# Optimization experiments

Hardware: AMD Instinct MI355X
Metric: run time of the kernel (lower is better)

The kernel has to match this reference:

```python
import jax, jax.numpy as jnp
import numpy as np

VOCAB = 100000
HID = 256
BATCH = 4096
TOTAL_TOKENS = 819200
BN_EPS = 1e-5


def setup_inputs() -> dict:
    key = jax.random.key(0)
    ks = jax.random.split(key, 8)
    token_ids = jax.random.randint(ks[0], (TOTAL_TOKENS,), 0, VOCAB, dtype=jnp.int64)
    segment_ids = jnp.sort(jax.random.randint(ks[1], (TOTAL_TOKENS,), 0, BATCH, dtype=jnp.int64))
    labels = jax.random.uniform(ks[2], (BATCH,), dtype=jnp.float32)
    emb = jax.random.normal(ks[3], (VOCAB, HID), dtype=jnp.float32)
    W1 = jax.random.normal(ks[4], (HID, HID), dtype=jnp.float32) * (1.0 / np.sqrt(HID))
    b1 = jnp.zeros((HID,), dtype=jnp.float32)
    gamma = jnp.ones((HID,), dtype=jnp.float32)
    beta = jnp.zeros((HID,), dtype=jnp.float32)
    W2 = jax.random.normal(ks[5], (1, HID), dtype=jnp.float32) * (1.0 / np.sqrt(HID))
    b2 = jnp.zeros((1,), dtype=jnp.float32)
    return {"token_ids": token_ids, "segment_ids": segment_ids, "labels": labels,
            "emb": emb, "W1": W1, "b1": b1, "gamma": gamma, "beta": beta,
            "W2": W2, "b2": b2}


def reference(token_ids, segment_ids, labels, emb, W1, b1, gamma, beta, W2, b2):
    # Ragged embedding gather + per-document mean (fused EmbeddingBag-mean).
    tok_emb = emb[token_ids]                                   # [T, H]
    seg_sum = jax.ops.segment_sum(tok_emb, segment_ids, num_segments=BATCH)  # [B, H]
    counts = jax.ops.segment_sum(jnp.ones((token_ids.shape[0],), tok_emb.dtype),
                                 segment_ids, num_segments=BATCH)            # [B]
    bow = seg_sum / jnp.maximum(counts, 1.0)[:, None]          # [B, H]
    # Linear -> BatchNorm1d (batch stats, biased var) -> ReLU
    h = bow @ W1.T + b1                                        # [B, H]
    mu = jnp.mean(h, axis=0)
    var = jnp.mean((h - mu) ** 2, axis=0)
    h = (h - mu) * jax.lax.rsqrt(var + BN_EPS) * gamma + beta
    h = jax.nn.relu(h)
    # Dropout in eval mode (identity) for deterministic reference.
    logits = (h @ W2.T + b2)[:, 0]                             # [B]
    # BCEWithLogitsLoss (mean), numerically stable form.
    loss = jnp.mean(jnp.maximum(logits, 0.0) - logits * labels
                    + jnp.log1p(jnp.exp(-jnp.abs(logits))))
    return (loss, logits)
```

## Files before the change

### kernel.cpp

```cpp
#include <hip/hip_runtime.h>
#include <math.h>

#define VOCAB 100000
#define HID 256
#define BATCH 4096
#define BN_EPS 1e-5f
#define TPB1 512
#define ROWS2 8

#define WS_SEGSUM 0
#define WS_COUNTS (BATCH * HID)
#define WS_COLSUM (WS_COUNTS + BATCH)
#define WS_COLSQ  (WS_COLSUM + HID)
#define WS_ZERO_FLOATS (WS_COLSQ + HID)

__global__ __launch_bounds__(256) void k1_gather_segsum(
    const int* __restrict__ token_ids, const int* __restrict__ segment_ids,
    const float* __restrict__ emb, float* __restrict__ seg_sum,
    float* __restrict__ counts, int T)
{
    __shared__ int s_tok[TPB1];
    __shared__ int s_seg[TPB1];
    const int tid  = threadIdx.x;
    const int t0   = blockIdx.x * TPB1;
    const int n    = min(TPB1, T - t0);
    if (n <= 0) return;
    for (int i = tid; i < n; i += 256) {
        s_tok[i] = token_ids[t0 + i];
        s_seg[i] = segment_ids[t0 + i];
    }
    __syncthreads();

    const int wave = tid >> 6;
    const int lane = tid & 63;
    const int per  = TPB1 / 4;
    const int start = wave * per;
    const int end   = min(start + per, n);
    if (start >= end) return;

    const float4* __restrict__ embv = reinterpret_cast<const float4*>(emb);
    float4 acc = make_float4(0.f, 0.f, 0.f, 0.f);
    int cur = s_seg[start];
    int runlen = 0;

#define K1_FLUSH() do {                                                        \
        float* p = &seg_sum[(size_t)cur * HID + lane * 4];                     \
        atomicAdd(p + 0, acc.x); atomicAdd(p + 1, acc.y);                      \
        atomicAdd(p + 2, acc.z); atomicAdd(p + 3, acc.w);                      \
        if (lane == 0) atomicAdd(&counts[cur], (float)runlen);                 \
        acc = make_float4(0.f, 0.f, 0.f, 0.f); runlen = 0;                     \
    } while (0)

#define K1_PROC(ii, v) do {                                                    \
        int seg = s_seg[ii];                  \
        if (seg != cur) { K1_FLUSH(); cur = seg; }                             \
        acc.x += (v).x; acc.y += (v).y; acc.z += (v).z; acc.w += (v).w;        \
        runlen++;                                                              \
    } while (0)

    const int m4 = start + ((end - start) & ~3);
    for (int i = start; i < m4; i += 4) {
        float4 a0 = embv[(size_t)s_tok[i + 0] * (HID / 4) + lane];
        float4 a1 = embv[(size_t)s_tok[i + 1] * (HID / 4) + lane];
        float4 a2 = embv[(size_t)s_tok[i + 2] * (HID / 4) + lane];
        float4 a3 = embv[(size_t)s_tok[i + 3] * (HID / 4) + lane];
        K1_PROC(i + 0, a0);
        K1_PROC(i + 1, a1);
        K1_PROC(i + 2, a2);
        K1_PROC(i + 3, a3);
    }
    for (int i = m4; i < end; ++i) {
        float4 a = embv[(size_t)s_tok[i] * (HID / 4) + lane];
        K1_PROC(i, a);
    }
    K1_FLUSH();
#undef K1_PROC
#undef K1_FLUSH
}

__global__ __launch_bounds__(256) void k2_gemm_bn_partial(
    const float* seg_sum, const float* __restrict__ counts,
    const float* __restrict__ W1, const float* __restrict__ b1,
    float* hout, float* __restrict__ colsum, float* __restrict__ colsq,
    float* __restrict__ out)
{
    __shared__ float s_bow[ROWS2][HID];
    const int tid = threadIdx.x;
    const int b0  = blockIdx.x * ROWS2;

    if (blockIdx.x == 0 && tid == 0) out[0] = 0.f;

#pragma unroll
    for (int r = 0; r < ROWS2; ++r) {
        float c   = counts[b0 + r];
        float inv = 1.f / fmaxf(c, 1.f);
        s_bow[r][tid] = seg_sum[(size_t)(b0 + r) * HID + tid] * inv;
    }
    __syncthreads();

    const int j = tid;
    float acc[ROWS2];
    const float bj = b1[j];
#pragma unroll
    for (int r = 0; r < ROWS2; ++r) acc[r] = bj;

    const float4* W1v = reinterpret_cast<const float4*>(W1 + (size_t)j * HID);
#pragma unroll 4
    for (int k4 = 0; k4 < HID / 4; ++k4) {
        float4 w = W1v[k4];
#pragma unroll
        for (int r = 0; r < ROWS2; ++r) {
            const float4* bv = reinterpret_cast<const float4*>(&s_bow[r][0]);
            float4 bb = bv[k4];
            acc[r] = fmaf(bb.x, w.x, acc[r]);
            acc[r] = fmaf(bb.y, w.y, acc[r]);
            acc[r] = fmaf(bb.z, w.z, acc[r]);
            acc[r] = fmaf(bb.w, w.w, acc[r]);
        }
    }

    float ls = 0.f, lq = 0.f;
#pragma unroll
    for (int r = 0; r < ROWS2; ++r) {
        float v = acc[r];
        hout[(size_t)(b0 + r) * HID + j] = v;
        ls += v;
        lq += v * v;
    }
    atomicAdd(&colsum[j], ls);
    atomicAdd(&colsq[j], lq);
}

__global__ __launch_bounds__(256) void k5_bn_relu_logits_loss(
    const float* __restrict__ hmat,
    const float* __restrict__ colsum, const float* __restrict__ colsq,
    const float* __restrict__ gamma, const float* __restrict__ beta,
    const float* __restrict__ W2, const float* __restrict__ b2,
    const float* __restrict__ labels, float* __restrict__ out)
{
    __shared__ float s_loss[4];
    const int tid  = threadIdx.x;
    const int w    = tid >> 6;
    const int lane = tid & 63;
    const int b0   = blockIdx.x * 16 + w * 4;

    const int j0 = lane, j1 = lane + 64, j2 = lane + 128, j3 = lane + 192;

#define BN_SS(jj, sc, sh) \
    { float mu = colsum[jj] * (1.f / BATCH); \
      float vr = colsq[jj] * (1.f / BATCH) - mu * mu; \
      sc = gamma[jj] * rsqrtf(vr + BN_EPS); \
      sh = beta[jj] - mu * sc; }
    float sc0, sh0, sc1, sh1, sc2, sh2, sc3, sh3;
    BN_SS(j0, sc0, sh0); BN_SS(j1, sc1, sh1);
    BN_SS(j2, sc2, sh2); BN_SS(j3, sc3, sh3);
#undef BN_SS

    const float w0 = W2[j0], w1 = W2[j1], w2v = W2[j2], w3 = W2[j3];
    const float bias2 = b2[0];

    float bce_acc = 0.f;
#pragma unroll
    for (int rr = 0; rr < 4; ++rr) {
        const int b = b0 + rr;
        const float* hr = hmat + (size_t)b * HID;
        float h0 = hr[j0], h1 = hr[j1], h2 = hr[j2], h3 = hr[j3];
        float s = 0.f;
        s += fmaxf(fmaf(h0, sc0, sh0), 0.f) * w0;
        s += fmaxf(fmaf(h1, sc1, sh1), 0.f) * w1;
        s += fmaxf(fmaf(h2, sc2, sh2), 0.f) * w2v;
        s += fmaxf(fmaf(h3, sc3, sh3), 0.f) * w3;
#pragma unroll
        for (int off = 32; off > 0; off >>= 1)
            s += __shfl_down(s, off, 64);
        if (lane == 0) {
            float z = s + bias2;
            out[1 + b] = z;
            float lb = labels[b];
            bce_acc += fmaxf(z, 0.f) - z * lb + log1pf(expf(-fabsf(z)));
        }
    }
    if (lane == 0) s_loss[w] = bce_acc;
    __syncthreads();
    if (tid == 0) {
        float t = (s_loss[0] + s_loss[1]) + (s_loss[2] + s_loss[3]);
        atomicAdd(&out[0], t * (1.f / BATCH));
    }
}

extern "C" void kernel_launch(void* const* d_in, const int* in_sizes, int n_in,
                              void* d_out, int out_size, void* d_ws, size_t ws_size,
                              hipStream_t stream)
{
    const int*   token_ids   = (const int*)d_in[0];
    const int*   segment_ids = (const int*)d_in[1];
    const float* labels      = (const float*)d_in[2];
    const float* emb         = (const float*)d_in[3];
    const float* W1          = (const float*)d_in[4];
    const float* b1          = (const float*)d_in[5];
    const float* gamma       = (const float*)d_in[6];
    const float* beta        = (const float*)d_in[7];
    const float* W2          = (const float*)d_in[8];
    const float* b2          = (const float*)d_in[9];
    float* out = (float*)d_out;
    float* ws  = (float*)d_ws;

    float* seg_sum = ws + WS_SEGSUM;
    float* counts  = ws + WS_COUNTS;
    float* colsum  = ws + WS_COLSUM;
    float* colsq   = ws + WS_COLSQ;

    const int T = in_sizes[0];

    hipMemsetAsync(d_ws, 0, (size_t)WS_ZERO_FLOATS * sizeof(float), stream);

    const int g1 = (T + TPB1 - 1) / TPB1;
    k1_gather_segsum<<<g1, 256, 0, stream>>>(token_ids, segment_ids, emb,
                                             seg_sum, counts, T);
    k2_gemm_bn_partial<<<BATCH / ROWS2, 256, 0, stream>>>(
        seg_sum, counts, W1, b1, seg_sum, colsum, colsq, out);
    k5_bn_relu_logits_loss<<<BATCH / 16, 256, 0, stream>>>(
        seg_sum, colsum, colsq, gamma, beta, W2, b2, labels, out);
}
```

Baseline: 312.6 us.

## Convert embedding table to fp16 per call and gather halves; tile W1 via shared memory

Each call now runs a kernel that converts the fp32 embedding table to fp16 in workspace, and the gather reads 8-byte half rows with 8-way unrolled loads, accumulating in fp32. This halves the gather bytes per token but adds a full read of the table and a half-size write on every call. The GEMM kernel also stages W1 in transposed K-tiles in shared memory with register prefetch, replacing per-thread strided row reads. A fallback keeps the fp32 gather when the workspace is too small.

```diff
diff --git a/kernel.cpp b/kernel.cpp
--- a/kernel.cpp
+++ b/kernel.cpp
@@ -1,4 +1,5 @@
 #include <hip/hip_runtime.h>
+#include <hip/hip_fp16.h>
 #include <math.h>
 
 #define VOCAB 100000
@@ -7,23 +8,40 @@
 #define BN_EPS 1e-5f
 #define TPB1 512
 #define ROWS2 8
+#define KT 16
 
 #define WS_SEGSUM 0
 #define WS_COUNTS (BATCH * HID)
 #define WS_COLSUM (WS_COUNTS + BATCH)
 #define WS_COLSQ  (WS_COLSUM + HID)
 #define WS_ZERO_FLOATS (WS_COLSQ + HID)
-
-__global__ __launch_bounds__(256) void k1_gather_segsum(
+#define WS_EMB16_OFF_BYTES ((size_t)WS_ZERO_FLOATS * 4)
+#define WS_FP16_BYTES_NEEDED (WS_EMB16_OFF_BYTES + (size_t)VOCAB * HID * 2)
+
+__global__ __launch_bounds__(256) void k0_convert(
+    const float* __restrict__ emb, __half* __restrict__ emb16, int n4)
+{
+    int i = blockIdx.x * 256 + threadIdx.x;
+    if (i >= n4) return;
+    float4 v = reinterpret_cast<const float4*>(emb)[i];
+    __half2 a = __halves2half2(__float2half_rn(v.x), __float2half_rn(v.y));
+    __half2 b = __halves2half2(__float2half_rn(v.z), __float2half_rn(v.w));
+    uint2 o;
+    o.x = __builtin_bit_cast(unsigned int, a);
+    o.y = __builtin_bit_cast(unsigned int, b);
+    reinterpret_cast<uint2*>(emb16)[i] = o;
+}
+
+__global__ __launch_bounds__(256) void k1_gather_fp16(
     const int* __restrict__ token_ids, const int* __restrict__ segment_ids,
-    const float* __restrict__ emb, float* __restrict__ seg_sum,
+    const __half* __restrict__ emb16, float* __restrict__ seg_sum,
     float* __restrict__ counts, int T)
 {
     __shared__ int s_tok[TPB1];
     __shared__ int s_seg[TPB1];
-    const int tid  = threadIdx.x;
-    const int t0   = blockIdx.x * TPB1;
-    const int n    = min(TPB1, T - t0);
+    const int tid = threadIdx.x;
+    const int t0  = blockIdx.x * TPB1;
+    const int n   = min(TPB1, T - t0);
     if (n <= 0) return;
     for (int i = tid; i < n; i += 256) {
         s_tok[i] = token_ids[t0 + i];
@@ -38,7 +56,7 @@
     const int end   = min(start + per, n);
     if (start >= end) return;
 
-    const float4* __restrict__ embv = reinterpret_cast<const float4*>(emb);
+    const uint2* __restrict__ embv = reinterpret_cast<const uint2*>(emb16);
     float4 acc = make_float4(0.f, 0.f, 0.f, 0.f);
     int cur = s_seg[start];
     int runlen = 0;
@@ -51,8 +69,80 @@
         acc = make_float4(0.f, 0.f, 0.f, 0.f); runlen = 0;                     \
     } while (0)
 
+#define K1_PROC16(ii, u) do {                                                  \
+        int seg = s_seg[ii];                  \
+        if (seg != cur) { K1_FLUSH(); cur = seg; }                             \
+        __half2 h01 = __builtin_bit_cast(__half2, (u).x);                      \
+        __half2 h23 = __builtin_bit_cast(__half2, (u).y);                      \
+        float2 f01 = __half22float2(h01);                                      \
+        float2 f23 = __half22float2(h23);                                      \
+        acc.x += f01.x; acc.y += f01.y; acc.z += f23.x; acc.w += f23.y;        \
+        runlen++;                                                              \
+    } while (0)
+
+    const int m8 = start + ((end - start) & ~7);
+    for (int i = start; i < m8; i += 8) {
+        uint2 u0 = embv[(size_t)s_tok[i + 0] * 64 + lane];
+        uint2 u1 = embv[(size_t)s_tok[i + 1] * 64 + lane];
+        uint2 u2 = embv[(size_t)s_tok[i + 2] * 64 + lane];
+        uint2 u3 = embv[(size_t)s_tok[i + 3] * 64 + lane];
+        uint2 u4 = embv[(size_t)s_tok[i + 4] * 64 + lane];
+        uint2 u5 = embv[(size_t)s_tok[i + 5] * 64 + lane];
+        uint2 u6 = embv[(size_t)s_tok[i + 6] * 64 + lane];
+        uint2 u7 = embv[(size_t)s_tok[i + 7] * 64 + lane];
+        K1_PROC16(i + 0, u0); K1_PROC16(i + 1, u1);
+        K1_PROC16(i + 2, u2); K1_PROC16(i + 3, u3);
+        K1_PROC16(i + 4, u4); K1_PROC16(i + 5, u5);
+        K1_PROC16(i + 6, u6); K1_PROC16(i + 7, u7);
+    }
+    for (int i = m8; i < end; ++i) {
+        uint2 u = embv[(size_t)s_tok[i] * 64 + lane];
+        K1_PROC16(i, u);
+    }
+    K1_FLUSH();
+#undef K1_PROC16
+#undef K1_FLUSH
+}
+
+__global__ __launch_bounds__(256) void k1_gather_fp32(
+    const int* __restrict__ token_ids, const int* __restrict__ segment_ids,
+    const float* __restrict__ emb, float* __restrict__ seg_sum,
+    float* __restrict__ counts, int T)
+{
+    __shared__ int s_tok[TPB1];
+    __shared__ int s_seg[TPB1];
+    const int tid = threadIdx.x;
+    const int t0  = blockIdx.x * TPB1;
+    const int n   = min(TPB1, T - t0);
+    if (n <= 0) return;
+    for (int i = tid; i < n; i += 256) {
+        s_tok[i] = token_ids[t0 + i];
+        s_seg[i] = segment_ids[t0 + i];
+    }
+    __syncthreads();
+
+    const int wave = tid >> 6;
+    const int lane = tid & 63;
+    const int per  = TPB1 / 4;
+    const int start = wave * per;
+    const int end   = min(start + per, n);
+    if (start >= end) return;
+
+    const float4* __restrict__ embv = reinterpret_cast<const float4*>(emb);
+    float4 acc = make_float4(0.f, 0.f, 0.f, 0.f);
+    int cur = s_seg[start];
+    int runlen = 0;
+
+#define K1_FLUSH() do {                                                        \
+        float* p = &seg_sum[(size_t)cur * HID + lane * 4];                     \
+        atomicAdd(p + 0, acc.x); atomicAdd(p + 1, acc.y);                      \
+        atomicAdd(p + 2, acc.z); atomicAdd(p + 3, acc.w);                      \
+        if (lane == 0) atomicAdd(&counts[cur], (float)runlen);                 \
+        acc = make_float4(0.f, 0.f, 0.f, 0.f); runlen = 0;                     \
+    } while (0)
+
 #define K1_PROC(ii, v) do {                                                    \
-        int seg = s_seg[ii];                  \
+        int seg = s_seg[ii];                                                   \
         if (seg != cur) { K1_FLUSH(); cur = seg; }                             \
         acc.x += (v).x; acc.y += (v).y; acc.z += (v).z; acc.w += (v).w;        \
         runlen++;                                                              \
@@ -60,17 +150,15 @@
 
     const int m4 = start + ((end - start) & ~3);
     for (int i = start; i < m4; i += 4) {
-        float4 a0 = embv[(size_t)s_tok[i + 0] * (HID / 4) + lane];
-        float4 a1 = embv[(size_t)s_tok[i + 1] * (HID / 4) + lane];
-        float4 a2 = embv[(size_t)s_tok[i + 2] * (HID / 4) + lane];
-        float4 a3 = embv[(size_t)s_tok[i + 3] * (HID / 4) + lane];
-        K1_PROC(i + 0, a0);
-        K1_PROC(i + 1, a1);
-        K1_PROC(i + 2, a2);
-        K1_PROC(i + 3, a3);
+        float4 a0 = embv[(size_t)s_tok[i + 0] * 64 + lane];
+        float4 a1 = embv[(size_t)s_tok[i + 1] * 64 + lane];
+        float4 a2 = embv[(size_t)s_tok[i + 2] * 64 + lane];
+        float4 a3 = embv[(size_t)s_tok[i + 3] * 64 + lane];
+        K1_PROC(i + 0, a0); K1_PROC(i + 1, a1);
+        K1_PROC(i + 2, a2); K1_PROC(i + 3, a3);
     }
     for (int i = m4; i < end; ++i) {
-        float4 a = embv[(size_t)s_tok[i] * (HID / 4) + lane];
+        float4 a = embv[(size_t)s_tok[i] * 64 + lane];
         K1_PROC(i, a);
     }
     K1_FLUSH();
@@ -85,6 +173,7 @@
     float* __restrict__ out)
 {
     __shared__ float s_bow[ROWS2][HID];
+    __shared__ float s_w1t[KT][HID + 1];
     const int tid = threadIdx.x;
     const int b0  = blockIdx.x * ROWS2;
 
@@ -96,26 +185,52 @@
         float inv = 1.f / fmaxf(c, 1.f);
         s_bow[r][tid] = seg_sum[(size_t)(b0 + r) * HID + tid] * inv;
     }
-    __syncthreads();
-
-    const int j = tid;
+
+    const int jrow = tid >> 2;
+    const int kq   = tid & 3;
+    const float4* __restrict__ W1v4 = reinterpret_cast<const float4*>(W1);
+
     float acc[ROWS2];
-    const float bj = b1[j];
+    const float bj = b1[tid];
 #pragma unroll
     for (int r = 0; r < ROWS2; ++r) acc[r] = bj;
 
-    const float4* W1v = reinterpret_cast<const float4*>(W1 + (size_t)j * HID);
-#pragma unroll 4
-    for (int k4 = 0; k4 < HID / 4; ++k4) {
-        float4 w = W1v[k4];
-#pragma unroll
-        for (int r = 0; r < ROWS2; ++r) {
-            const float4* bv = reinterpret_cast<const float4*>(&s_bow[r][0]);
-            float4 bb = bv[k4];
-            acc[r] = fmaf(bb.x, w.x, acc[r]);
-            acc[r] = fmaf(bb.y, w.y, acc[r]);
-            acc[r] = fmaf(bb.z, w.z, acc[r]);
-            acc[r] = fmaf(bb.w, w.w, acc[r]);
+    float4 pre[4];
+#pragma unroll
+    for (int p = 0; p < 4; ++p)
+        pre[p] = W1v4[(size_t)(p * 64 + jrow) * 64 + kq];
+
+    for (int kt = 0; kt < HID / KT; ++kt) {
+        __syncthreads();
+#pragma unroll
+        for (int p = 0; p < 4; ++p) {
+            int j = p * 64 + jrow;
+            s_w1t[kq * 4 + 0][j] = pre[p].x;
+            s_w1t[kq * 4 + 1][j] = pre[p].y;
+            s_w1t[kq * 4 + 2][j] = pre[p].z;
+            s_w1t[kq * 4 + 3][j] = pre[p].w;
+        }
+        __syncthreads();
+        if (kt + 1 < HID / KT) {
+#pragma unroll
+            for (int p = 0; p < 4; ++p)
+                pre[p] = W1v4[(size_t)(p * 64 + jrow) * 64 + (kt + 1) * 4 + kq];
+        }
+#pragma unroll
+        for (int q = 0; q < 4; ++q) {
+            float w0 = s_w1t[q * 4 + 0][tid];
+            float w1 = s_w1t[q * 4 + 1][tid];
+            float w2 = s_w1t[q * 4 + 2][tid];
+            float w3 = s_w1t[q * 4 + 3][tid];
+#pragma unroll
+            for (int r = 0; r < ROWS2; ++r) {
+                float4 bb = *reinterpret_cast<const float4*>(
+                    &s_bow[r][kt * KT + q * 4]);
+                acc[r] = fmaf(bb.x, w0,
+                         fmaf(bb.y, w1,
+                         fmaf(bb.z, w2,
+                         fmaf(bb.w, w3, acc[r]))));
+            }
         }
     }
 
@@ -123,12 +238,12 @@
 #pragma unroll
     for (int r = 0; r < ROWS2; ++r) {
         float v = acc[r];
-        hout[(size_t)(b0 + r) * HID + j] = v;
+        hout[(size_t)(b0 + r) * HID + tid] = v;
         ls += v;
         lq += v * v;
     }
-    atomicAdd(&colsum[j], ls);
-    atomicAdd(&colsq[j], lq);
+    atomicAdd(&colsum[tid], ls);
+    atomicAdd(&colsq[tid], lq);
 }
 
 __global__ __launch_bounds__(256) void k5_bn_relu_logits_loss(
@@ -211,12 +326,20 @@
     float* colsq   = ws + WS_COLSQ;
 
     const int T = in_sizes[0];
+    const int g1 = (T + TPB1 - 1) / TPB1;
 
     hipMemsetAsync(d_ws, 0, (size_t)WS_ZERO_FLOATS * sizeof(float), stream);
 
-    const int g1 = (T + TPB1 - 1) / TPB1;
-    k1_gather_segsum<<<g1, 256, 0, stream>>>(token_ids, segment_ids, emb,
-                                             seg_sum, counts, T);
+    if (ws_size >= WS_FP16_BYTES_NEEDED) {
+        __half* emb16 = (__half*)((char*)d_ws + WS_EMB16_OFF_BYTES);
+        const int n4 = VOCAB * HID / 4;
+        k0_convert<<<(n4 + 255) / 256, 256, 0, stream>>>(emb, emb16, n4);
+        k1_gather_fp16<<<g1, 256, 0, stream>>>(token_ids, segment_ids, emb16,
+                                               seg_sum, counts, T);
+    } else {
+        k1_gather_fp32<<<g1, 256, 0, stream>>>(token_ids, segment_ids, emb,
+                                               seg_sum, counts, T);
+    }
     k2_gemm_bn_partial<<<BATCH / ROWS2, 256, 0, stream>>>(
         seg_sum, counts, W1, b1, seg_sum, colsum, colsq, out);
     k5_bn_relu_logits_loss<<<BATCH / 16, 256, 0, stream>>>(
```

Result: faster. 284.2 us (-9.1%).
